# Performance work log

Hardware: AMD Instinct MI355X
Metric: run time of the kernel (lower is better)

## Reference

```python
import jax, jax.numpy as jnp
import numpy as np

N = 384
C_Z = 128
N_HEADS = 4
HEAD_DIM = C_Z // N_HEADS
LN_EPS = 1e-5


def _layernorm(x, w, b):
    mu = jnp.mean(x, axis=-1, keepdims=True)
    var = jnp.mean(jnp.square(x - mu), axis=-1, keepdims=True)
    return (x - mu) * jax.lax.rsqrt(var + LN_EPS) * w + b


def setup_inputs() -> dict:
    key = jax.random.key(0)
    ks = jax.random.split(key, 6)
    z = jax.random.normal(ks[0], (N, N, C_Z), dtype=jnp.float32)
    # Linear weights stored as [in, out] (transposed vs torch) so y = x @ W + b
    qkv_w = jax.random.normal(ks[1], (C_Z, 3 * C_Z), dtype=jnp.float32) * 0.02
    qkv_b = jnp.zeros((3 * C_Z,), dtype=jnp.float32)
    out_w = jax.random.normal(ks[2], (C_Z, C_Z), dtype=jnp.float32) * 0.02
    out_b = jnp.zeros((C_Z,), dtype=jnp.float32)
    gate_w = jax.random.normal(ks[3], (C_Z, C_Z), dtype=jnp.float32) * 0.02
    gate_b = jnp.zeros((C_Z,), dtype=jnp.float32)
    ln_w = jnp.ones((C_Z,), dtype=jnp.float32)
    ln_b = jnp.zeros((C_Z,), dtype=jnp.float32)
    return {"z": z, "ln_w": ln_w, "ln_b": ln_b, "qkv_w": qkv_w, "qkv_b": qkv_b,
            "out_w": out_w, "out_b": out_b, "gate_w": gate_w, "gate_b": gate_b}


def reference(z, ln_w, ln_b, qkv_w, qkv_b, out_w, out_b, gate_w, gate_b):
    # mode == 'starting': no transpose
    z_norm = _layernorm(z, ln_w, ln_b)                      # [N, N, c_z]
    qkv = (z_norm @ qkv_w + qkv_b).reshape(N, N, 3, N_HEADS, HEAD_DIM)
    q, k, v = qkv[:, :, 0], qkv[:, :, 1], qkv[:, :, 2]      # each [N, N, h, d]
    scale = 1.0 / np.sqrt(HEAD_DIM).astype(np.float32)
    attn = jnp.einsum('inhd,jnhd->nijh', q, k) * scale      # [N, N, N, h]
    attn = jax.nn.softmax(attn, axis=1)                     # softmax over i (dim=1)
    out = jnp.einsum('nijh,jnhd->inhd', attn, v)            # [N, N, h, d]
    out = out.reshape(N, N, C_Z)
    gate = jax.nn.sigmoid(z_norm @ gate_w + gate_b)
    return z + gate * (out @ out_w + out_b)
```

## Files before the change

kernel.cpp:

```cpp
#include <hip/hip_runtime.h>
#include <hip/hip_bf16.h>

#define NN 384
#define CZ 128
#define NH 4
#define HD 32
#define MROWS (NN*NN)

typedef __hip_bfloat16 bf16;
typedef short bf16x8f __attribute__((ext_vector_type(8)));
typedef float f32x4 __attribute__((ext_vector_type(4)));
typedef unsigned short u16x8 __attribute__((ext_vector_type(8)));
typedef unsigned int uint4v __attribute__((ext_vector_type(4)));

__device__ __forceinline__ float b2f(unsigned short u) {
    return __uint_as_float(((unsigned)u) << 16);
}
__device__ __forceinline__ unsigned short f2b(float f) {
    unsigned u = __float_as_uint(f);
    return (unsigned short)((u + 0x7FFFu + ((u >> 16) & 1u)) >> 16);
}
__device__ __forceinline__ unsigned cvt_pk_bf16(float lo, float hi) {
    unsigned r;
    asm("v_cvt_pk_bf16_f32 %0, %1, %2" : "=v"(r) : "v"(lo), "v"(hi));
    return r;
}
__device__ __forceinline__ float fexp2(float x) {
    float r;
    asm("v_exp_f32 %0, %1" : "=v"(r) : "v"(x));
    return r;
}

__global__ __launch_bounds__(256) void ln_stats_kernel(const float* __restrict__ z,
                                                       float* __restrict__ mu,
                                                       float* __restrict__ rstd) {
    const int wave = threadIdx.x >> 6;
    const int lane = threadIdx.x & 63;
    const int r = blockIdx.x * 4 + wave;
    const float* zr = z + (size_t)r * CZ;
    float x0 = zr[lane], x1 = zr[lane + 64];
    float sum = x0 + x1;
    float sq  = x0 * x0 + x1 * x1;
    #pragma unroll
    for (int o = 32; o > 0; o >>= 1) {
        sum += __shfl_xor(sum, o, 64);
        sq  += __shfl_xor(sq,  o, 64);
    }
    if (lane == 0) {
        const float m   = sum * (1.0f / CZ);
        const float var = sq * (1.0f / CZ) - m * m;
        mu[r]   = m;
        rstd[r] = rsqrtf(var + 1e-5f);
    }
}

__global__ __launch_bounds__(256) void qkv_gemm_mfma_kernel(const float* __restrict__ z,
                                                            const float* __restrict__ mu,
                                                            const float* __restrict__ rstd,
                                                            const float* __restrict__ lnw,
                                                            const float* __restrict__ lnb,
                                                            const float* __restrict__ W,
                                                            const float* __restrict__ bias,
                                                            unsigned short* __restrict__ qkv_t) {
    __shared__ unsigned short Zt[128 * 128];

    const int tid = threadIdx.x;
    const int w = tid >> 6;
    const int l = tid & 63;
    const int bid = blockIdx.x;
    const int xcd = bid & 7;
    const int idx = bid >> 3;
    const int yt  = idx / 6;
    const int x   = idx - yt * 6;
    const int col0 = x * 64;
    const int row0 = (xcd * 144 + yt) * 128;
    const int wcol = w & 1;
    const int wrow = w >> 1;
    const int lm = l & 15;
    const int lq = l >> 4;

    #pragma unroll
    for (int it = 0; it < 8; it++) {
        const int s = it * 256 + tid;
        const int r = s >> 4;
        const int c = (s & 15) ^ (r & 7);
        const int k0 = c * 8;
        const int grow = row0 + r;
        const float m  = mu[grow];
        const float rs = rstd[grow];
        const float4 z0 = *(const float4*)(z + (size_t)grow * CZ + k0);
        const float4 z1 = *(const float4*)(z + (size_t)grow * CZ + k0 + 4);
        const float4 w0 = *(const float4*)(lnw + k0);
        const float4 w1 = *(const float4*)(lnw + k0 + 4);
        const float4 b0 = *(const float4*)(lnb + k0);
        const float4 b1 = *(const float4*)(lnb + k0 + 4);
        u16x8 pk;
        pk[0] = f2b((z0.x - m) * rs * w0.x + b0.x);
        pk[1] = f2b((z0.y - m) * rs * w0.y + b0.y);
        pk[2] = f2b((z0.z - m) * rs * w0.z + b0.z);
        pk[3] = f2b((z0.w - m) * rs * w0.w + b0.w);
        pk[4] = f2b((z1.x - m) * rs * w1.x + b1.x);
        pk[5] = f2b((z1.y - m) * rs * w1.y + b1.y);
        pk[6] = f2b((z1.z - m) * rs * w1.z + b1.z);
        pk[7] = f2b((z1.w - m) * rs * w1.w + b1.w);
        *(u16x8*)&Zt[s * 8] = pk;
    }

    bf16x8f a[2][4];
    #pragma unroll
    for (int fm = 0; fm < 2; fm++) {
        const int gcol = col0 + wcol * 32 + fm * 16 + lm;
        #pragma unroll
        for (int kk = 0; kk < 4; kk++) {
            const int kb = kk * 32 + lq * 8;
            #pragma unroll
            for (int j = 0; j < 8; j++)
                a[fm][kk][j] = (short)f2b(W[(size_t)(kb + j) * (3 * CZ) + gcol]);
        }
    }

    __syncthreads();

    f32x4 acc[2][4];
    #pragma unroll
    for (int fm = 0; fm < 2; fm++)
        #pragma unroll
        for (int fn = 0; fn < 4; fn++)
            acc[fm][fn] = (f32x4){0.0f, 0.0f, 0.0f, 0.0f};

    #pragma unroll
    for (int kk = 0; kk < 4; kk++) {
        bf16x8f bf[4];
        #pragma unroll
        for (int fn = 0; fn < 4; fn++) {
            const int r = wrow * 64 + fn * 16 + lm;
            const int ch = (kk * 4 + lq) ^ (r & 7);
            bf[fn] = *(const bf16x8f*)&Zt[(r * 16 + ch) * 8];
        }
        #pragma unroll
        for (int fm = 0; fm < 2; fm++)
            #pragma unroll
            for (int fn = 0; fn < 4; fn++)
                acc[fm][fn] = __builtin_amdgcn_mfma_f32_16x16x32_bf16(a[fm][kk], bf[fn],
                                                                      acc[fm][fn], 0, 0, 0);
    }

    #pragma unroll
    for (int fm = 0; fm < 2; fm++) {
        const int gc = col0 + wcol * 32 + fm * 16 + lq * 4;
        const float4 b4 = *(const float4*)(bias + gc);
        const int t  = gc >> 7;
        const int hh = (gc & 127) >> 5;
        const int d0 = gc & 31;
        const size_t colbase = (size_t)((t * NH + hh) * NN) * (NN * HD) + d0;
        #pragma unroll
        for (int fn = 0; fn < 4; fn++) {
            const int grow = row0 + wrow * 64 + fn * 16 + lm;
            const int i  = grow / NN;
            const int n0 = grow - i * NN;
            const size_t idx2 = colbase + (size_t)n0 * (NN * HD) + (size_t)i * HD;
            ushort4 pk;
            pk.x = f2b(acc[fm][fn][0] + b4.x);
            pk.y = f2b(acc[fm][fn][1] + b4.y);
            pk.z = f2b(acc[fm][fn][2] + b4.z);
            pk.w = f2b(acc[fm][fn][3] + b4.w);
            *(ushort4*)(qkv_t + idx2) = pk;
        }
    }
}

__global__ __launch_bounds__(256) void attn_mfma_kernel(const unsigned short* __restrict__ qkv_t,
                                                        float* __restrict__ attn_out) {
    __shared__ unsigned short Kf[24 * 512];
    __shared__ unsigned short Vf[2][1024];
    __shared__ float sred[2][4][32];

    const int b = blockIdx.x;
    const int n = b >> 2;
    const int h = b & 3;
    const int tid = threadIdx.x;
    const int w = tid >> 6;
    const int l = tid & 63;
    const int q = l >> 4;
    const int m = l & 15;
    const size_t base_q = (size_t)((0 * NH + h) * NN + n) * (NN * HD);
    const size_t base_k = (size_t)((1 * NH + h) * NN + n) * (NN * HD);
    const size_t base_v = (size_t)((2 * NH + h) * NN + n) * (NN * HD);
    const float SC2 = 0.17677669529663687f * 1.4426950408889634f;
    const f32x4 zero = {0.0f, 0.0f, 0.0f, 0.0f};

    #pragma unroll
    for (int it = 0; it < 6; it++) {
        const int slot = tid + it * 256;
        const int t  = slot >> 6;
        const int l2 = slot & 63;
        const int row = t * 16 + (l2 & 15);
        const int off8 = (l2 >> 4) * 8;
        *(u16x8*)(Kf + slot * 8) =
            *(const u16x8*)(qkv_t + base_k + (size_t)row * HD + off8);
    }
    bf16x8f qreg[6];
    #pragma unroll
    for (int tt = 0; tt < 6; tt++) {
        const int row = (w + 4 * tt) * 16 + m;
        qreg[tt] = *(const bf16x8f*)(qkv_t + base_q + (size_t)row * HD + q * 8);
    }
    __syncthreads();

    f32x4 oacc[6][2];
    #pragma unroll
    for (int tt = 0; tt < 6; tt++) {
        oacc[tt][0] = zero;
        oacc[tt][1] = zero;
    }

    unsigned pawA[6][4], pawB[6][4];
    const int jj  = tid >> 3;
    const int d0v = (tid & 7) * 4;
    const int slotbase = (d0v >> 4) * 64 + (jj >> 3) * 16 + (d0v & 15);
    const int e = jj & 7;

    #pragma unroll
    for (int cl = 0; cl < 12; cl++) {
        const int buf = cl & 1;
        const bf16x8f ka0 = *(const bf16x8f*)&Kf[(cl * 2 + 0) * 512 + l * 8];
        const bf16x8f ka1 = *(const bf16x8f*)&Kf[(cl * 2 + 1) * 512 + l * 8];
        const ushort4 v4 = *(const ushort4*)(qkv_t + base_v +
                                             (size_t)(cl * 32 + jj) * HD + d0v);

        float sacc[8];
        #pragma unroll
        for (int k = 0; k < 8; k++) sacc[k] = 0.0f;

        #pragma unroll
        for (int tt = 0; tt < 6; tt++) {
            const f32x4 sT0 = __builtin_amdgcn_mfma_f32_16x16x32_bf16(ka0, qreg[tt], zero, 0, 0, 0);
            const f32x4 sT1 = __builtin_amdgcn_mfma_f32_16x16x32_bf16(ka1, qreg[tt], zero, 0, 0, 0);
            float p[8];
            p[0] = fexp2(sT0[0] * SC2);
            p[1] = fexp2(sT0[1] * SC2);
            p[2] = fexp2(sT0[2] * SC2);
            p[3] = fexp2(sT0[3] * SC2);
            p[4] = fexp2(sT1[0] * SC2);
            p[5] = fexp2(sT1[1] * SC2);
            p[6] = fexp2(sT1[2] * SC2);
            p[7] = fexp2(sT1[3] * SC2);
            #pragma unroll
            for (int k = 0; k < 8; k++) sacc[k] += p[k];
            unsigned c0 = cvt_pk_bf16(p[0], p[1]);
            unsigned c1 = cvt_pk_bf16(p[2], p[3]);
            unsigned c2 = cvt_pk_bf16(p[4], p[5]);
            unsigned c3 = cvt_pk_bf16(p[6], p[7]);
            asm("v_permlane32_swap_b32 %0, %1" : "+v"(c0), "+v"(c2));
            asm("v_permlane32_swap_b32 %0, %1" : "+v"(c1), "+v"(c3));
            asm("v_permlane16_swap_b32 %0, %1" : "+v"(c0), "+v"(c2));
            asm("v_permlane16_swap_b32 %0, %1" : "+v"(c1), "+v"(c3));
            if (buf == 0) {
                pawA[tt][0] = c0; pawA[tt][1] = c1; pawA[tt][2] = c2; pawA[tt][3] = c3;
            } else {
                pawB[tt][0] = c0; pawB[tt][1] = c1; pawB[tt][2] = c2; pawB[tt][3] = c3;
            }
        }

        #pragma unroll
        for (int k = 0; k < 8; k++) {
            float v = sacc[k];
            v += __shfl_xor(v, 1, 64);
            v += __shfl_xor(v, 2, 64);
            v += __shfl_xor(v, 4, 64);
            v += __shfl_xor(v, 8, 64);
            if (m == 0) sred[buf][w][q * 4 + (k & 3) + (k >> 2) * 16] = v;
        }
        __syncthreads();

        {
            const float inv = 1.0f / (sred[buf][0][jj] + sred[buf][1][jj] +
                                      sred[buf][2][jj] + sred[buf][3][jj]);
            Vf[buf][(slotbase + 0) * 8 + e] = f2b(b2f(v4.x) * inv);
            Vf[buf][(slotbase + 1) * 8 + e] = f2b(b2f(v4.y) * inv);
            Vf[buf][(slotbase + 2) * 8 + e] = f2b(b2f(v4.z) * inv);
            Vf[buf][(slotbase + 3) * 8 + e] = f2b(b2f(v4.w) * inv);
        }

        if (cl > 0) {
            const bf16x8f vb0 = *(const bf16x8f*)&Vf[buf ^ 1][(0 * 64 + l) * 8];
            const bf16x8f vb1 = *(const bf16x8f*)&Vf[buf ^ 1][(1 * 64 + l) * 8];
            #pragma unroll
            for (int tt = 0; tt < 6; tt++) {
                uint4v u;
                if (buf == 1) { u = (uint4v){pawA[tt][0], pawA[tt][1], pawA[tt][2], pawA[tt][3]}; }
                else          { u = (uint4v){pawB[tt][0], pawB[tt][1], pawB[tt][2], pawB[tt][3]}; }
                const bf16x8f pa = __builtin_bit_cast(bf16x8f, u);
                oacc[tt][0] = __builtin_amdgcn_mfma_f32_16x16x32_bf16(pa, vb0, oacc[tt][0], 0, 0, 0);
                oacc[tt][1] = __builtin_amdgcn_mfma_f32_16x16x32_bf16(pa, vb1, oacc[tt][1], 0, 0, 0);
            }
        }
    }

    __syncthreads();
    {
        const bf16x8f vb0 = *(const bf16x8f*)&Vf[1][(0 * 64 + l) * 8];
        const bf16x8f vb1 = *(const bf16x8f*)&Vf[1][(1 * 64 + l) * 8];
        #pragma unroll
        for (int tt = 0; tt < 6; tt++) {
            const uint4v u = {pawB[tt][0], pawB[tt][1], pawB[tt][2], pawB[tt][3]};
            const bf16x8f pa = __builtin_bit_cast(bf16x8f, u);
            oacc[tt][0] = __builtin_amdgcn_mfma_f32_16x16x32_bf16(pa, vb0, oacc[tt][0], 0, 0, 0);
            oacc[tt][1] = __builtin_amdgcn_mfma_f32_16x16x32_bf16(pa, vb1, oacc[tt][1], 0, 0, 0);
        }
    }

    #pragma unroll
    for (int tt = 0; tt < 6; tt++) {
        const int it = w + 4 * tt;
        #pragma unroll
        for (int dt = 0; dt < 2; dt++) {
            #pragma unroll
            for (int r = 0; r < 4; r++) {
                const int i = it * 16 + q * 4 + r;
                attn_out[((size_t)i * NN + n) * CZ + h * HD + dt * 16 + m] = oacc[tt][dt][r];
            }
        }
    }
}

__global__ __launch_bounds__(256) void final_mfma_kernel(const float* __restrict__ z,
                                                         const float* __restrict__ mu,
                                                         const float* __restrict__ rstd,
                                                         const float* __restrict__ lnw,
                                                         const float* __restrict__ lnb,
                                                         const float* __restrict__ gate_w,
                                                         const float* __restrict__ gate_b,
                                                         const float* __restrict__ out_w,
                                                         const float* __restrict__ out_b,
                                                         float* out) {
    __shared__ unsigned short Zt[64 * 128];
    __shared__ unsigned short At[64 * 128];

    const int tid = threadIdx.x;
    const int w = tid >> 6;
    const int l = tid & 63;
    const int lm = l & 15;
    const int lq = l >> 4;
    const int row0 = blockIdx.x * 64;

    #pragma unroll
    for (int it = 0; it < 4; it++) {
        const int s = it * 256 + tid;
        const int r = s >> 4;
        const int c = (s & 15) ^ (r & 7);
        const int k0 = c * 8;
        const int grow = row0 + r;
        const float m  = mu[grow];
        const float rs = rstd[grow];
        const size_t gi = (size_t)grow * CZ + k0;
        const float4 z0 = *(const float4*)(z + gi);
        const float4 z1 = *(const float4*)(z + gi + 4);
        const float4 a0 = *(const float4*)(out + gi);
        const float4 a1 = *(const float4*)(out + gi + 4);
        const float4 w0 = *(const float4*)(lnw + k0);
        const float4 w1 = *(const float4*)(lnw + k0 + 4);
        const float4 b0 = *(const float4*)(lnb + k0);
        const float4 b1 = *(const float4*)(lnb + k0 + 4);
        u16x8 pz, pa;
        pz[0] = f2b((z0.x - m) * rs * w0.x + b0.x);
        pz[1] = f2b((z0.y - m) * rs * w0.y + b0.y);
        pz[2] = f2b((z0.z - m) * rs * w0.z + b0.z);
        pz[3] = f2b((z0.w - m) * rs * w0.w + b0.w);
        pz[4] = f2b((z1.x - m) * rs * w1.x + b1.x);
        pz[5] = f2b((z1.y - m) * rs * w1.y + b1.y);
        pz[6] = f2b((z1.z - m) * rs * w1.z + b1.z);
        pz[7] = f2b((z1.w - m) * rs * w1.w + b1.w);
        pa[0] = f2b(a0.x); pa[1] = f2b(a0.y); pa[2] = f2b(a0.z); pa[3] = f2b(a0.w);
        pa[4] = f2b(a1.x); pa[5] = f2b(a1.y); pa[6] = f2b(a1.z); pa[7] = f2b(a1.w);
        *(u16x8*)&Zt[s * 8] = pz;
        *(u16x8*)&At[s * 8] = pa;
    }

    bf16x8f gw[2][4], ow[2][4];
    #pragma unroll
    for (int fm = 0; fm < 2; fm++) {
        const int gcol = w * 32 + fm * 16 + lm;
        #pragma unroll
        for (int kk = 0; kk < 4; kk++) {
            const int kb = kk * 32 + lq * 8;
            #pragma unroll
            for (int j = 0; j < 8; j++) {
                gw[fm][kk][j] = (short)f2b(gate_w[(size_t)(kb + j) * CZ + gcol]);
                ow[fm][kk][j] = (short)f2b(out_w [(size_t)(kb + j) * CZ + gcol]);
            }
        }
    }

    __syncthreads();

    f32x4 acc1[2][4], acc2[2][4];
    #pragma unroll
    for (int fm = 0; fm < 2; fm++)
        #pragma unroll
        for (int fn = 0; fn < 4; fn++) {
            acc1[fm][fn] = (f32x4){0.0f, 0.0f, 0.0f, 0.0f};
            acc2[fm][fn] = (f32x4){0.0f, 0.0f, 0.0f, 0.0f};
        }

    #pragma unroll
    for (int kk = 0; kk < 4; kk++) {
        bf16x8f bz[4], ba[4];
        #pragma unroll
        for (int fn = 0; fn < 4; fn++) {
            const int r = fn * 16 + lm;
            const int ch = (kk * 4 + lq) ^ (r & 7);
            bz[fn] = *(const bf16x8f*)&Zt[(r * 16 + ch) * 8];
            ba[fn] = *(const bf16x8f*)&At[(r * 16 + ch) * 8];
        }
        #pragma unroll
        for (int fm = 0; fm < 2; fm++)
            #pragma unroll
            for (int fn = 0; fn < 4; fn++) {
                acc1[fm][fn] = __builtin_amdgcn_mfma_f32_16x16x32_bf16(gw[fm][kk], bz[fn],
                                                                       acc1[fm][fn], 0, 0, 0);
                acc2[fm][fn] = __builtin_amdgcn_mfma_f32_16x16x32_bf16(ow[fm][kk], ba[fn],
                                                                       acc2[fm][fn], 0, 0, 0);
            }
    }

    #pragma unroll
    for (int fm = 0; fm < 2; fm++) {
        const int gc = w * 32 + fm * 16 + lq * 4;
        const float4 gb4 = *(const float4*)(gate_b + gc);
        const float4 ob4 = *(const float4*)(out_b + gc);
        #pragma unroll
        for (int fn = 0; fn < 4; fn++) {
            const int grow = row0 + fn * 16 + lm;
            const size_t idx = (size_t)grow * CZ + gc;
            const float4 z4 = *(const float4*)(z + idx);
            float4 o;
            o.x = z4.x + (1.0f / (1.0f + __expf(-(acc1[fm][fn][0] + gb4.x)))) * (acc2[fm][fn][0] + ob4.x);
            o.y = z4.y + (1.0f / (1.0f + __expf(-(acc1[fm][fn][1] + gb4.y)))) * (acc2[fm][fn][1] + ob4.y);
            o.z = z4.z + (1.0f / (1.0f + __expf(-(acc1[fm][fn][2] + gb4.z)))) * (acc2[fm][fn][2] + ob4.z);
            o.w = z4.w + (1.0f / (1.0f + __expf(-(acc1[fm][fn][3] + gb4.w)))) * (acc2[fm][fn][3] + ob4.w);
            *(float4*)(out + idx) = o;
        }
    }
}

extern "C" void kernel_launch(void* const* d_in, const int* in_sizes, int n_in,
                              void* d_out, int out_size, void* d_ws, size_t ws_size,
                              hipStream_t stream) {
    const float* z      = (const float*)d_in[0];
    const float* ln_w   = (const float*)d_in[1];
    const float* ln_b   = (const float*)d_in[2];
    const float* qkv_w  = (const float*)d_in[3];
    const float* qkv_b  = (const float*)d_in[4];
    const float* out_w  = (const float*)d_in[5];
    const float* out_b  = (const float*)d_in[6];
    const float* gate_w = (const float*)d_in[7];
    const float* gate_b = (const float*)d_in[8];
    float* out = (float*)d_out;

    float* ws = (float*)d_ws;
    float* mu_buf   = ws;
    float* rstd_buf = ws + MROWS;
    unsigned short* qkv_t = (unsigned short*)(ws + 2 * MROWS);

    ln_stats_kernel<<<MROWS / 4, 256, 0, stream>>>(z, mu_buf, rstd_buf);
    qkv_gemm_mfma_kernel<<<6912, 256, 0, stream>>>(z, mu_buf, rstd_buf,
                                                   ln_w, ln_b, qkv_w, qkv_b, qkv_t);
    attn_mfma_kernel<<<NN * NH, 256, 0, stream>>>(qkv_t, out);
    final_mfma_kernel<<<MROWS / 64, 256, 0, stream>>>(z, mu_buf, rstd_buf, ln_w, ln_b,
                                                      gate_w, gate_b, out_w, out_b, out);
}
```

Before: 391.2 us.

## Pre-transpose weights to bf16 and materialize layernormed z once

Adds a small prep kernel that converts and transposes qkv, gate and out weights to bf16 [out,in] layout, so GEMM kernels load weight fragments with single vector loads instead of strided scalar fp32 loads plus conversion. The stats kernel now also writes the normalized z in bf16 into the output buffer as scratch, and the QKV GEMM copies tiles directly instead of re-normalizing fp32 z. This trades an extra bf16 write/read pass for halving the GEMM's input traffic and removing redundant per-block weight conversion. It relies on attn output overwriting the scratch region before the final kernel reads it.

```diff
diff --git a/kernel.cpp b/kernel.cpp
--- a/kernel.cpp
+++ b/kernel.cpp
@@ -31,14 +31,30 @@
     return r;
 }
 
-__global__ __launch_bounds__(256) void ln_stats_kernel(const float* __restrict__ z,
+__global__ __launch_bounds__(128) void prep_w_kernel(const float* __restrict__ qkv_w,
+                                                     const float* __restrict__ gate_w,
+                                                     const float* __restrict__ out_w,
+                                                     unsigned short* __restrict__ Wt) {
+    const int cid = blockIdx.x;
+    const int k   = threadIdx.x;
+    float v;
+    if (cid < 384)      v = qkv_w [(size_t)k * (3 * CZ) + cid];
+    else if (cid < 512) v = gate_w[(size_t)k * CZ + (cid - 384)];
+    else                v = out_w [(size_t)k * CZ + (cid - 512)];
+    Wt[(size_t)cid * CZ + k] = f2b(v);
+}
+
+__global__ __launch_bounds__(256) void ln_apply_kernel(const float* __restrict__ z,
+                                                       const float* __restrict__ lnw,
+                                                       const float* __restrict__ lnb,
                                                        float* __restrict__ mu,
-                                                       float* __restrict__ rstd) {
+                                                       float* __restrict__ rstd,
+                                                       unsigned short* __restrict__ lnz) {
     const int wave = threadIdx.x >> 6;
     const int lane = threadIdx.x & 63;
     const int r = blockIdx.x * 4 + wave;
     const float* zr = z + (size_t)r * CZ;
-    float x0 = zr[lane], x1 = zr[lane + 64];
+    const float x0 = zr[lane], x1 = zr[lane + 64];
     float sum = x0 + x1;
     float sq  = x0 * x0 + x1 * x1;
     #pragma unroll
@@ -46,20 +62,20 @@
         sum += __shfl_xor(sum, o, 64);
         sq  += __shfl_xor(sq,  o, 64);
     }
+    const float m  = sum * (1.0f / CZ);
+    const float rs = rsqrtf(sq * (1.0f / CZ) - m * m + 1e-5f);
     if (lane == 0) {
-        const float m   = sum * (1.0f / CZ);
-        const float var = sq * (1.0f / CZ) - m * m;
         mu[r]   = m;
-        rstd[r] = rsqrtf(var + 1e-5f);
-    }
-}
-
-__global__ __launch_bounds__(256) void qkv_gemm_mfma_kernel(const float* __restrict__ z,
-                                                            const float* __restrict__ mu,
-                                                            const float* __restrict__ rstd,
-                                                            const float* __restrict__ lnw,
-                                                            const float* __restrict__ lnb,
-                                                            const float* __restrict__ W,
+        rstd[r] = rs;
+    }
+    const float w0 = lnw[lane], w1 = lnw[lane + 64];
+    const float b0 = lnb[lane], b1 = lnb[lane + 64];
+    lnz[(size_t)r * CZ + lane]      = f2b((x0 - m) * rs * w0 + b0);
+    lnz[(size_t)r * CZ + lane + 64] = f2b((x1 - m) * rs * w1 + b1);
+}
+
+__global__ __launch_bounds__(256) void qkv_gemm_mfma_kernel(const unsigned short* __restrict__ lnz,
+                                                            const unsigned short* __restrict__ Wt,
                                                             const float* __restrict__ bias,
                                                             unsigned short* __restrict__ qkv_t) {
     __shared__ unsigned short Zt[128 * 128];
@@ -83,27 +99,9 @@
     for (int it = 0; it < 8; it++) {
         const int s = it * 256 + tid;
         const int r = s >> 4;
-        const int c = (s & 15) ^ (r & 7);
-        const int k0 = c * 8;
-        const int grow = row0 + r;
-        const float m  = mu[grow];
-        const float rs = rstd[grow];
-        const float4 z0 = *(const float4*)(z + (size_t)grow * CZ + k0);
-        const float4 z1 = *(const float4*)(z + (size_t)grow * CZ + k0 + 4);
-        const float4 w0 = *(const float4*)(lnw + k0);
-        const float4 w1 = *(const float4*)(lnw + k0 + 4);
-        const float4 b0 = *(const float4*)(lnb + k0);
-        const float4 b1 = *(const float4*)(lnb + k0 + 4);
-        u16x8 pk;
-        pk[0] = f2b((z0.x - m) * rs * w0.x + b0.x);
-        pk[1] = f2b((z0.y - m) * rs * w0.y + b0.y);
-        pk[2] = f2b((z0.z - m) * rs * w0.z + b0.z);
-        pk[3] = f2b((z0.w - m) * rs * w0.w + b0.w);
-        pk[4] = f2b((z1.x - m) * rs * w1.x + b1.x);
-        pk[5] = f2b((z1.y - m) * rs * w1.y + b1.y);
-        pk[6] = f2b((z1.z - m) * rs * w1.z + b1.z);
-        pk[7] = f2b((z1.w - m) * rs * w1.w + b1.w);
-        *(u16x8*)&Zt[s * 8] = pk;
+        const int cc = (s & 15) ^ (r & 7);
+        *(u16x8*)&Zt[s * 8] =
+            *(const u16x8*)(lnz + (size_t)(row0 + r) * CZ + cc * 8);
     }
 
     bf16x8f a[2][4];
@@ -111,12 +109,8 @@
     for (int fm = 0; fm < 2; fm++) {
         const int gcol = col0 + wcol * 32 + fm * 16 + lm;
         #pragma unroll
-        for (int kk = 0; kk < 4; kk++) {
-            const int kb = kk * 32 + lq * 8;
-            #pragma unroll
-            for (int j = 0; j < 8; j++)
-                a[fm][kk][j] = (short)f2b(W[(size_t)(kb + j) * (3 * CZ) + gcol]);
-        }
+        for (int kk = 0; kk < 4; kk++)
+            a[fm][kk] = *(const bf16x8f*)(Wt + (size_t)gcol * CZ + kk * 32 + lq * 8);
     }
 
     __syncthreads();
@@ -329,9 +323,9 @@
                                                          const float* __restrict__ rstd,
                                                          const float* __restrict__ lnw,
                                                          const float* __restrict__ lnb,
-                                                         const float* __restrict__ gate_w,
+                                                         const unsigned short* __restrict__ Gt,
                                                          const float* __restrict__ gate_b,
-                                                         const float* __restrict__ out_w,
+                                                         const unsigned short* __restrict__ Ot,
                                                          const float* __restrict__ out_b,
                                                          float* out) {
     __shared__ unsigned short Zt[64 * 128];
@@ -384,11 +378,8 @@
         #pragma unroll
         for (int kk = 0; kk < 4; kk++) {
             const int kb = kk * 32 + lq * 8;
-            #pragma unroll
-            for (int j = 0; j < 8; j++) {
-                gw[fm][kk][j] = (short)f2b(gate_w[(size_t)(kb + j) * CZ + gcol]);
-                ow[fm][kk][j] = (short)f2b(out_w [(size_t)(kb + j) * CZ + gcol]);
-            }
+            gw[fm][kk] = *(const bf16x8f*)(Gt + (size_t)gcol * CZ + kb);
+            ow[fm][kk] = *(const bf16x8f*)(Ot + (size_t)gcol * CZ + kb);
         }
     }
 
@@ -461,12 +452,16 @@
     float* ws = (float*)d_ws;
     float* mu_buf   = ws;
     float* rstd_buf = ws + MROWS;
-    unsigned short* qkv_t = (unsigned short*)(ws + 2 * MROWS);
-
-    ln_stats_kernel<<<MROWS / 4, 256, 0, stream>>>(z, mu_buf, rstd_buf);
-    qkv_gemm_mfma_kernel<<<6912, 256, 0, stream>>>(z, mu_buf, rstd_buf,
-                                                   ln_w, ln_b, qkv_w, qkv_b, qkv_t);
+    unsigned short* Wt    = (unsigned short*)(ws + 2 * MROWS);
+    unsigned short* Gt    = Wt + 384 * CZ;
+    unsigned short* Ot    = Wt + 512 * CZ;
+    unsigned short* qkv_t = Wt + 640 * CZ;
+    unsigned short* lnz = (unsigned short*)out;
+
+    prep_w_kernel<<<640, 128, 0, stream>>>(qkv_w, gate_w, out_w, Wt);
+    ln_apply_kernel<<<MROWS / 4, 256, 0, stream>>>(z, ln_w, ln_b, mu_buf, rstd_buf, lnz);
+    qkv_gemm_mfma_kernel<<<6912, 256, 0, stream>>>(lnz, Wt, qkv_b, qkv_t);
     attn_mfma_kernel<<<NN * NH, 256, 0, stream>>>(qkv_t, out);
     final_mfma_kernel<<<MROWS / 64, 256, 0, stream>>>(z, mu_buf, rstd_buf, ln_w, ln_b,
-                                                      gate_w, gate_b, out_w, out_b, out);
-}
+                                                      Gt, gate_b, Ot, out_b, out);
+}
```

Measured after the change: 368.5 us. -5.8%, faster.
